# Kernel optimization log

Measured on AMD Instinct MI355X. Metric: run time of the kernel, lower is better.

Reference implementation:

```python
import jax, jax.numpy as jnp
import numpy as np

K = 3  # kernel_size hard-coded in MorphologicalLoss
DICE_W, BOUND_W, MORPH_W = 0.3, 0.2, 0.2


def _kernel_mask():
    c = K // 2
    y, x = np.meshgrid(np.arange(K), np.arange(K), indexing='ij')
    m = ((x - c) ** 2 + (y - c) ** 2 <= c ** 2).astype(np.float32)  # circular (cross) SE
    return jnp.asarray(m.reshape(-1))  # [K*K]


def _patches(x):
    # x: [B,1,H,W] -> [B,1,K*K,H,W] (same as F.unfold with padding=K//2)
    p = K // 2
    xp = jnp.pad(x, ((0, 0), (0, 0), (p, p), (p, p)))
    H, W = x.shape[2], x.shape[3]
    views = [xp[:, :, dy:dy + H, dx:dx + W] for dy in range(K) for dx in range(K)]
    return jnp.stack(views, axis=2)


def _dilation(x, mask):
    m = mask.reshape(1, 1, -1, 1, 1)
    comp = (1.0 - _patches(x)) * m + (1.0 - m)
    return jnp.clip(1.0 - jnp.prod(comp, axis=2), 0.0, 1.0)


def _erosion(x, mask):
    m = mask.reshape(1, 1, -1, 1, 1)
    nb = _patches(x) * m + (1.0 - m)
    return jnp.clip(jnp.prod(nb, axis=2), 0.0, 1.0)


def _l1(a, b):
    return jnp.mean(jnp.abs(a - b))


def _loss(pred, target):
    mask = _kernel_mask()
    # reconstruction (l1)
    total = _l1(pred, target)
    # dice
    smooth = 1e-05
    inter = jnp.sum(pred * target)
    union = jnp.sum(pred) + jnp.sum(target)
    dice = jnp.clip((2.0 * inter + smooth) / (union + smooth), 0.0, 1.0)
    total = total + DICE_W * (-jnp.log(dice + 1e-08))
    # boundary gradients
    pgx = jnp.abs(pred[:, :, :, 1:] - pred[:, :, :, :-1])
    pgy = jnp.abs(pred[:, :, 1:, :] - pred[:, :, :-1, :])
    tgx = jnp.abs(target[:, :, :, 1:] - target[:, :, :, :-1])
    tgy = jnp.abs(target[:, :, 1:, :] - target[:, :, :-1, :])
    total = total + BOUND_W * 0.5 * (_l1(pgx, tgx) + _l1(pgy, tgy))
    # morphological consistency
    dil_loss = _l1(_dilation(pred, mask), _dilation(target, mask))
    ero_loss = _l1(_erosion(pred, mask), _erosion(target, mask))
    total = total + MORPH_W * 0.5 * (dil_loss + ero_loss)
    return jnp.maximum(total, 0.0)


def setup_inputs() -> dict:
    key = jax.random.key(0)
    k1, k2 = jax.random.split(key)
    B, C, H, W = 32, 1, 512, 512
    pred = jax.random.uniform(k1, (B, C, H, W), dtype=jnp.float32)
    target = jax.random.uniform(k2, (B, C, H, W), dtype=jnp.float32)
    return {"pred": pred, "target": target}


def reference(pred, target):
    return _loss(pred, target)
```

## Files before the change

kernel.cpp:

```cpp
#include <hip/hip_runtime.h>
#include <math.h>

constexpr int IMG_W  = 512;
constexpr int IMG_H  = 512;
constexpr int BATCH  = 32;
constexpr int NPIX   = BATCH * IMG_H * IMG_W;
constexpr int NROWS  = BATCH * IMG_H;
constexpr int BROWS  = 64;
constexpr int NTHR   = 512;
constexpr int NBLK   = NROWS / BROWS;
constexpr int NXCD   = 8;
constexpr int NACC   = 8;

__device__ __forceinline__ void row_compute(
    const float4& pU, const float4& tU,
    const float4& pC, const float4& tC,
    const float4& pD, const float4& tD,
    int gi, int lane128, int lane64, bool gyok,
    const float* __restrict__ pred, const float* __restrict__ tgt,
    float* a)
{
    float pl = __shfl_up(pC.w, 1, 64);
    float tl = __shfl_up(tC.w, 1, 64);
    float pr = __shfl_down(pC.x, 1, 64);
    float tr = __shfl_down(tC.x, 1, 64);
    if (lane64 == 0) {
        if (lane128 == 0) { pl = 0.f; tl = 0.f; }
        else              { pl = pred[gi - 1]; tl = tgt[gi - 1]; }
    }
    if (lane64 == 63) {
        if (lane128 == 127) { pr = 0.f; tr = 0.f; }
        else                { pr = pred[gi + 4]; tr = tgt[gi + 4]; }
    }
    const bool hasR = (lane128 != 127);

    const float* pcA = &pC.x; const float* tcA = &tC.x;
    const float* ppA = &pU.x; const float* tpA = &tU.x;
    const float* pnA = &pD.x; const float* tnA = &tD.x;

#pragma unroll
    for (int j = 0; j < 4; ++j) {
        const float pcj = pcA[j], tcj = tcA[j];
        a[0] += fabsf(pcj - tcj);
        a[1] += pcj * tcj;
        a[2] += pcj;
        a[3] += tcj;
        if (j < 3)
            a[4] += fabsf(fabsf(pcA[j + 1] - pcj) - fabsf(tcA[j + 1] - tcj));
        const float plj = j ? pcA[j - 1] : pl;
        const float prj = (j < 3) ? pcA[j + 1] : pr;
        const float tlj = j ? tcA[j - 1] : tl;
        const float trj = (j < 3) ? tcA[j + 1] : tr;
        float dp = 1.f - (1.f - pcj) * (1.f - plj) * (1.f - prj) * (1.f - ppA[j]) * (1.f - pnA[j]);
        float dt = 1.f - (1.f - tcj) * (1.f - tlj) * (1.f - trj) * (1.f - tpA[j]) * (1.f - tnA[j]);
        dp = fminf(fmaxf(dp, 0.f), 1.f);
        dt = fminf(fmaxf(dt, 0.f), 1.f);
        a[6] += fabsf(dp - dt);
        float ep = pcj * plj * prj * ppA[j] * pnA[j];
        float et = tcj * tlj * trj * tpA[j] * tnA[j];
        ep = fminf(fmaxf(ep, 0.f), 1.f);
        et = fminf(fmaxf(et, 0.f), 1.f);
        a[7] += fabsf(ep - et);
    }
    if (hasR)
        a[4] += fabsf(fabsf(pr - pcA[3]) - fabsf(tr - tcA[3]));
    if (gyok) {
#pragma unroll
        for (int j = 0; j < 4; ++j)
            a[5] += fabsf(fabsf(pnA[j] - pcA[j]) - fabsf(tnA[j] - tcA[j]));
    }
}

__global__ __launch_bounds__(NTHR) void morph_partials(
    const float* __restrict__ pred, const float* __restrict__ tgt,
    float* __restrict__ ws)
{
    float a[NACC];
#pragma unroll
    for (int k = 0; k < NACC; ++k) a[k] = 0.f;

    const int swz = (blockIdx.x % NXCD) * (NBLK / NXCD) + blockIdx.x / NXCD;

    const int unit    = threadIdx.x >> 7;
    const int lane128 = threadIdx.x & 127;
    const int lane64  = threadIdx.x & 63;
    const bool down   = !(unit & 1);
    const int gb      = swz * BROWS;
    const int img     = gb >> 9;
    const int yb      = gb & 511;
    const int imgbase = (img << 18) + (lane128 << 2);

    __shared__ float4 xch[4][2][128];
    __shared__ float  smr[NACC][NTHR / 64];

    const float4 z4 = make_float4(0.f, 0.f, 0.f, 0.f);
    float4 pU = z4, tU = z4, pC, tC, pD = z4, tD = z4;

    const int yl0 = down ? unit * 16 : unit * 16 + 15;
    {
        const int idx = imgbase + ((yb + yl0) << 9);
        pC = *(const float4*)(pred + idx);
        tC = *(const float4*)(tgt  + idx);
    }
    xch[unit][0][lane128] = pC;
    xch[unit][1][lane128] = tC;
    __syncthreads();
    if (unit == 0) {
        if (yb != 0) {
            const int idx = imgbase + ((yb - 1) << 9);
            pU = *(const float4*)(pred + idx);
            tU = *(const float4*)(tgt  + idx);
        }
    } else if (unit == 1) {
        pD = xch[2][0][lane128]; tD = xch[2][1][lane128];
    } else if (unit == 2) {
        pU = xch[1][0][lane128]; tU = xch[1][1][lane128];
    } else {
        if (yb != IMG_H - BROWS) {
            const int idx = imgbase + ((yb + BROWS) << 9);
            pD = *(const float4*)(pred + idx);
            tD = *(const float4*)(tgt  + idx);
        }
    }

    for (int r = 0; r < 16; ++r) {
        const int yl = down ? unit * 16 + r : unit * 16 + 15 - r;
        const int yi = yb + yl;
        if (r == 15) {
            __syncthreads();
            xch[unit][0][lane128] = pC;
            xch[unit][1][lane128] = tC;
            __syncthreads();
            const int pair = unit ^ 1;
            if (down) { pD = xch[pair][0][lane128]; tD = xch[pair][1][lane128]; }
            else      { pU = xch[pair][0][lane128]; tU = xch[pair][1][lane128]; }
        } else {
            const int ny  = down ? yi + 1 : yi - 1;
            const int idx = imgbase + (ny << 9);
            if (down) { pD = *(const float4*)(pred + idx); tD = *(const float4*)(tgt + idx); }
            else      { pU = *(const float4*)(pred + idx); tU = *(const float4*)(tgt + idx); }
        }
        const bool gyok = (yi != IMG_H - 1);
        const int  gi   = imgbase + (yi << 9);
        row_compute(pU, tU, pC, tC, pD, tD, gi, lane128, lane64, gyok, pred, tgt, a);
        if (down) { pU = pC; tU = tC; pC = pD; tC = tD; }
        else      { pD = pC; tD = tC; pC = pU; tC = tU; }
    }

#pragma unroll
    for (int k = 0; k < NACC; ++k) {
        float v = a[k];
        for (int o = 32; o > 0; o >>= 1) v += __shfl_down(v, o, 64);
        if ((threadIdx.x & 63) == 0) smr[k][threadIdx.x >> 6] = v;
    }
    __syncthreads();
    if (threadIdx.x < NACC) {
        float v = 0.f;
#pragma unroll
        for (int w = 0; w < NTHR / 64; ++w) v += smr[threadIdx.x][w];
        ws[threadIdx.x * NBLK + blockIdx.x] = v;
    }
}

__global__ __launch_bounds__(256) void morph_final(
    const float* __restrict__ ws, float* __restrict__ out)
{
    __shared__ double sm[NACC][256 / 64];
#pragma unroll
    for (int k = 0; k < NACC; ++k) {
        double v = 0.0;
        for (int idx = threadIdx.x; idx < NBLK; idx += 256)
            v += (double)ws[k * NBLK + idx];
        for (int o = 32; o > 0; o >>= 1) v += __shfl_down(v, o, 64);
        if ((threadIdx.x & 63) == 0) sm[k][threadIdx.x >> 6] = v;
    }
    __syncthreads();
    if (threadIdx.x == 0) {
        double r[NACC];
#pragma unroll
        for (int k = 0; k < NACC; ++k) {
            double s = 0.0;
            for (int w = 0; w < 256 / 64; ++w) s += sm[k][w];
            r[k] = s;
        }
        const double Npix  = (double)NPIX;
        const double Ngrad = (double)BATCH * IMG_H * (IMG_W - 1);

        double total = r[0] / Npix;
        double dice = (2.0 * r[1] + 1e-5) / (r[2] + r[3] + 1e-5);
        dice = fmin(fmax(dice, 0.0), 1.0);
        total += 0.3 * (-log(dice + 1e-8));
        total += 0.2 * 0.5 * ((r[4] + r[5]) / Ngrad);
        total += 0.2 * 0.5 * ((r[6] + r[7]) / Npix);

        out[0] = (float)fmax(total, 0.0);
    }
}

extern "C" void kernel_launch(void* const* d_in, const int* in_sizes, int n_in,
                              void* d_out, int out_size, void* d_ws, size_t ws_size,
                              hipStream_t stream) {
    const float* pred = (const float*)d_in[0];
    const float* tgt  = (const float*)d_in[1];
    float* out = (float*)d_out;
    float* ws  = (float*)d_ws;

    morph_partials<<<NBLK, NTHR, 0, stream>>>(pred, tgt, ws);
    morph_final<<<1, 256, 0, stream>>>(ws, out);
}
```

Measured before the change: 29.90 us.

## Fuse final reduction into main kernel via atomics and last-block detection

Replaces the separate single-block final reduction kernel with float atomicAdds into eight global accumulators plus a block counter, so the last block to finish computes the loss. This removes one kernel launch and the partials write/read, but adds a memset before the launch and atomic contention on eight addresses. Accumulating in float atomics instead of a double sum changes summation order and precision.

```diff
diff --git a/kernel.cpp b/kernel.cpp
--- a/kernel.cpp
+++ b/kernel.cpp
@@ -71,9 +71,9 @@
     }
 }
 
-__global__ __launch_bounds__(NTHR) void morph_partials(
+__global__ __launch_bounds__(NTHR) void morph_fused(
     const float* __restrict__ pred, const float* __restrict__ tgt,
-    float* __restrict__ ws)
+    float* accum, unsigned int* counter, float* __restrict__ out)
 {
     float a[NACC];
 #pragma unroll
@@ -154,35 +154,30 @@
         if ((threadIdx.x & 63) == 0) smr[k][threadIdx.x >> 6] = v;
     }
     __syncthreads();
+
+    __shared__ bool isLast;
     if (threadIdx.x < NACC) {
         float v = 0.f;
 #pragma unroll
         for (int w = 0; w < NTHR / 64; ++w) v += smr[threadIdx.x][w];
-        ws[threadIdx.x * NBLK + blockIdx.x] = v;
-    }
-}
-
-__global__ __launch_bounds__(256) void morph_final(
-    const float* __restrict__ ws, float* __restrict__ out)
-{
-    __shared__ double sm[NACC][256 / 64];
-#pragma unroll
-    for (int k = 0; k < NACC; ++k) {
-        double v = 0.0;
-        for (int idx = threadIdx.x; idx < NBLK; idx += 256)
-            v += (double)ws[k * NBLK + idx];
-        for (int o = 32; o > 0; o >>= 1) v += __shfl_down(v, o, 64);
-        if ((threadIdx.x & 63) == 0) sm[k][threadIdx.x >> 6] = v;
-    }
+        atomicAdd(&accum[threadIdx.x], v);
+    }
+    if (threadIdx.x < 64)
+        asm volatile("s_waitcnt vmcnt(0)" ::: "memory");
+    if (threadIdx.x == 0)
+        isLast = (atomicAdd(counter, 1u) == NBLK - 1);
+    __syncthreads();
+    if (!isLast) return;
+
+    __shared__ float fin[NACC];
+    if (threadIdx.x < NACC)
+        fin[threadIdx.x] = atomicAdd(&accum[threadIdx.x], 0.0f);
     __syncthreads();
     if (threadIdx.x == 0) {
         double r[NACC];
 #pragma unroll
-        for (int k = 0; k < NACC; ++k) {
-            double s = 0.0;
-            for (int w = 0; w < 256 / 64; ++w) s += sm[k][w];
-            r[k] = s;
-        }
+        for (int k = 0; k < NACC; ++k) r[k] = (double)fin[k];
+
         const double Npix  = (double)NPIX;
         const double Ngrad = (double)BATCH * IMG_H * (IMG_W - 1);
 
@@ -203,8 +198,9 @@
     const float* pred = (const float*)d_in[0];
     const float* tgt  = (const float*)d_in[1];
     float* out = (float*)d_out;
-    float* ws  = (float*)d_ws;
-
-    morph_partials<<<NBLK, NTHR, 0, stream>>>(pred, tgt, ws);
-    morph_final<<<1, 256, 0, stream>>>(ws, out);
+    float* accum = (float*)d_ws;
+    unsigned int* counter = (unsigned int*)((char*)d_ws + 32);
+
+    hipMemsetAsync(d_ws, 0, 64, stream);
+    morph_fused<<<NBLK, NTHR, 0, stream>>>(pred, tgt, accum, counter, out);
 }
```

Measured after the change: 35.46 us. 1.19x slower.
